# Optimization experiments

Hardware: AMD Instinct MI355X
Metric: run time of the kernel (lower is better)

The kernel has to match this reference:

```python
import jax, jax.numpy as jnp
import numpy as np

SIGMA = 1.0  # init kwarg sigma

def _rbf_kernel(A):
    # K[i,j] = exp(-0.5 * ||a_i - a_j||^2 / sigma^2)
    sq = jnp.sum(A * A, axis=1)                      # [n]
    d2 = sq[:, None] + sq[None, :] - 2.0 * (A @ A.T)  # [n, n]
    return jnp.exp(-0.5 * d2 / (SIGMA ** 2))

def _double_center(K):
    # C K C with C = I - 11^T/n, done in O(n^2) via mean subtraction
    row = K.mean(axis=1, keepdims=True)
    col = K.mean(axis=0, keepdims=True)
    tot = K.mean()
    return K - row - col + tot

def setup_inputs() -> dict:
    key = jax.random.key(0)
    kx, ky = jax.random.split(key)
    X = jax.random.normal(kx, (4096, 512), dtype=jnp.float32)
    Y = jax.random.normal(ky, (4096, 512), dtype=jnp.float32)
    return {"X": X, "Y": Y}

def reference(X, Y):
    n = X.shape[0]
    KXc = _double_center(_rbf_kernel(X))
    KYc = _double_center(_rbf_kernel(Y))
    # trace(KX C KY C) = sum(center(KX) * center(KY)) since K symmetric, C idempotent
    hsic = jnp.sum(KXc * KYc) / ((n - 1) ** 2)
    return hsic
```

## Files before the change

### kernel.cpp

```cpp
#include <hip/hip_runtime.h>
#include <hip/hip_bf16.h>

namespace {

constexpr int N = 4096;
constexpr int D = 512;
constexpr int BM = 64;
constexpr int BK = 64;
constexpr int KITERS = D / BK;
constexpr int NB = N / BM;
constexpr int NBLK = NB * (NB + 1) / 2;
constexpr int TILEB = BM * BK;
constexpr int PANELB = BM * D;

constexpr size_t OFF_XB  = 0;
constexpr size_t OFF_YB  = (size_t)N * D;
constexpr size_t OFF_SQX = OFF_YB + (size_t)N * D;
constexpr size_t OFF_SQY = OFF_SQX + (size_t)N * 4;
constexpr size_t OFF_SX  = OFF_SQY + (size_t)N * 4;
constexpr size_t OFF_SY  = OFF_SX + (size_t)N * 4;
constexpr size_t OFF_T1  = OFF_SY + (size_t)N * 4;
constexpr size_t WS_NEED = OFF_T1 + 4;


constexpr float D2_SKIP = 240.f;

typedef __attribute__((ext_vector_type(4))) float floatx4;
typedef __attribute__((ext_vector_type(2))) long longx2;

__device__ inline void stage16(const void* g, void* l) {
  __builtin_amdgcn_global_load_lds(
      (const __attribute__((address_space(1))) unsigned int*)g,
      (__attribute__((address_space(3))) unsigned int*)l, 16, 0, 0);
}

__device__ inline unsigned short bf16bits(float f) {
  return __builtin_bit_cast(unsigned short, __float2bfloat16(f));
}

__global__ void prep_kernel(const float* __restrict__ X, const float* __restrict__ Y,
                            unsigned char* __restrict__ Xf8, unsigned char* __restrict__ Yf8,
                            float* __restrict__ sqX, float* __restrict__ sqY,
                            float* __restrict__ sX, float* __restrict__ sY,
                            float* __restrict__ T1) {
  const int wave = threadIdx.x >> 6, lane = threadIdx.x & 63;
  const int row = blockIdx.x * 4 + wave;
  const int m = blockIdx.y;
  const float* __restrict__ src = m ? Y : X;
  unsigned char* __restrict__ dst = m ? Yf8 : Xf8;
  float* __restrict__ dsq = m ? sqY : sqX;

  if (threadIdx.x < 4) {
    float* z = m ? sY : sX;
    z[blockIdx.x * 4 + threadIdx.x] = 0.f;
  }
  if (blockIdx.x == 0 && m == 0 && threadIdx.x == 0) *T1 = 0.f;

  const float4* s4 = (const float4*)(src + (size_t)row * D);
  float4 v0 = s4[lane * 2];
  float4 v1 = s4[lane * 2 + 1];
  float acc = v0.x * v0.x + v0.y * v0.y + v0.z * v0.z + v0.w * v0.w
            + v1.x * v1.x + v1.y * v1.y + v1.z * v1.z + v1.w * v1.w;

  unsigned int w0 = 0, w1 = 0;
  w0 = __builtin_amdgcn_cvt_pk_fp8_f32(v0.x, v0.y, w0, false);
  w0 = __builtin_amdgcn_cvt_pk_fp8_f32(v0.z, v0.w, w0, true);
  w1 = __builtin_amdgcn_cvt_pk_fp8_f32(v1.x, v1.y, w1, false);
  w1 = __builtin_amdgcn_cvt_pk_fp8_f32(v1.z, v1.w, w1, true);
  const unsigned long long pk =
      (unsigned long long)w0 | ((unsigned long long)w1 << 32);

  const int p    = row >> 6;
  const int nib  = (row >> 4) & 3;
  const int cl   = row & 15;
  const int ks   = lane >> 3;
  const int pass = (lane >> 2) & 1;
  const int quad = lane & 3;
  const size_t off = (size_t)p * PANELB + (size_t)ks * TILEB +
                     nib * 1024 + quad * 256 + cl * 16 + pass * 8;
  *(unsigned long long*)(dst + off) = pk;

#pragma unroll
  for (int mm = 32; mm >= 1; mm >>= 1) acc += __shfl_xor(acc, mm, 64);
  if (lane == 0) dsq[row] = acc;
}

__launch_bounds__(256, 4)
__global__ void hsic_main(const unsigned char* __restrict__ Xf8,
                          const unsigned char* __restrict__ Yf8,
                          const float* __restrict__ sqX, const float* __restrict__ sqY,
                          float* __restrict__ sX, float* __restrict__ sY,
                          float* __restrict__ T1) {
  __shared__ __align__(16) unsigned char smem[3][2 * TILEB];

  const int b = blockIdx.x;
  int idx = (b & 7) * (NBLK / 8) + (b >> 3);

  const float nf = (float)NB + 0.5f;
  int bI = (int)(nf - sqrtf(nf * nf - 2.0f * (float)idx));
  if (bI < 0) bI = 0;
  if (bI >= NB) bI = NB - 1;
  while (bI * NB - bI * (bI - 1) / 2 > idx) --bI;
  while ((bI + 1) * NB - (bI + 1) * bI / 2 <= idx) ++bI;
  const int bJ = bI + (idx - (bI * NB - bI * (bI - 1) / 2));
  const bool offdiag = (bI != bJ);

  const int tid = threadIdx.x;
  const int lane = tid & 63, wave = tid >> 6;
  const int wm = wave >> 1, wn = wave & 1;
  const int quad = lane >> 4, cl = lane & 15;

  const unsigned char* gAx = Xf8 + (size_t)bI * PANELB;
  const unsigned char* gBx = Xf8 + (size_t)bJ * PANELB;
  const unsigned char* gAy = Yf8 + (size_t)bI * PANELB;
  const unsigned char* gBy = Yf8 + (size_t)bJ * PANELB;

  floatx4 acc[2][2];
#pragma unroll
  for (int i = 0; i < 2; ++i)
#pragma unroll
    for (int j = 0; j < 2; ++j) acc[i][j] = (floatx4){0.f, 0.f, 0.f, 0.f};

  auto stage_all = [&](int iter, int buf) {
    const unsigned char* gA = (iter < KITERS) ? gAx : gAy;
    const unsigned char* gB = (iter < KITERS) ? gBx : gBy;
    const size_t goff = (size_t)(iter & (KITERS - 1)) * TILEB + (size_t)tid * 16;
    stage16(gA + goff, &smem[buf][0 * TILEB + tid * 16]);
    stage16(gB + goff, &smem[buf][1 * TILEB + tid * 16]);
  };

  const int Ib = bI * BM + wm * 32;
  const int Jb = bJ * BM + wn * 32;

  unsigned int kxp[2][2][2];
  unsigned int fmask = 0;
  float t1l = 0.f;

  stage_all(0, 0);
  stage_all(1, 1);

  for (int iter = 0; iter < 2 * KITERS; ++iter) {
    if (iter < 2 * KITERS - 1) {
      asm volatile("s_waitcnt vmcnt(2)" ::: "memory");
    } else {
      asm volatile("s_waitcnt vmcnt(0)" ::: "memory");
    }
    asm volatile("s_barrier" ::: "memory");
    if (iter + 2 < 2 * KITERS) stage_all(iter + 2, (iter + 2) % 3);

    const unsigned char* A = &smem[iter % 3][0];
    const unsigned char* B = &smem[iter % 3][TILEB];

    longx2 bf[2];
#pragma unroll
    for (int ni = 0; ni < 2; ++ni)
      bf[ni] = *(const longx2*)&B[(wn * 2 + ni) * 1024 + (lane << 4)];
#pragma unroll
    for (int mi = 0; mi < 2; ++mi) {
      const longx2 af = *(const longx2*)&A[(wm * 2 + mi) * 1024 + (lane << 4)];
#pragma unroll
      for (int ni = 0; ni < 2; ++ni) {
        acc[mi][ni] = __builtin_amdgcn_mfma_f32_16x16x32_fp8_fp8(af[0], bf[ni][0], acc[mi][ni], 0, 0, 0);
        acc[mi][ni] = __builtin_amdgcn_mfma_f32_16x16x32_fp8_fp8(af[1], bf[ni][1], acc[mi][ni], 0, 0, 0);
      }
    }

    if (iter == KITERS - 1) {
      float rx[2][4];
      float cx[2];
#pragma unroll
      for (int mi = 0; mi < 2; ++mi)
#pragma unroll
        for (int r = 0; r < 4; ++r) rx[mi][r] = 0.f;
#pragma unroll
      for (int ni = 0; ni < 2; ++ni) cx[ni] = 0.f;

#pragma unroll
      for (int mi = 0; mi < 2; ++mi) {
        const int ig0 = Ib + mi * 16 + quad * 4;
        float sxi[4];
#pragma unroll
        for (int r = 0; r < 4; ++r) sxi[r] = sqX[ig0 + r];
#pragma unroll
        for (int ni = 0; ni < 2; ++ni) {
          const int jg = Jb + ni * 16 + cl;
          const float sxj = sqX[jg];
          float d2x[4];
          bool lflag = false;
#pragma unroll
          for (int r = 0; r < 4; ++r) {
            const int ig = ig0 + r;
            d2x[r] = sxi[r] + sxj - 2.f * acc[mi][ni][r];
            lflag |= (d2x[r] < D2_SKIP) | (ig == jg);
          }
          float kxv[4] = {0.f, 0.f, 0.f, 0.f};
          if (__any(lflag)) {
            fmask |= (1u << (mi * 2 + ni));
#pragma unroll
            for (int r = 0; r < 4; ++r) {
              const int ig = ig0 + r;
              kxv[r] = (ig == jg) ? 1.f : __expf(-0.5f * d2x[r]);
              rx[mi][r] += kxv[r];
              cx[ni] += kxv[r];
            }
          }
          kxp[mi][ni][0] = (unsigned)bf16bits(kxv[0]) | ((unsigned)bf16bits(kxv[1]) << 16);
          kxp[mi][ni][1] = (unsigned)bf16bits(kxv[2]) | ((unsigned)bf16bits(kxv[3]) << 16);
          acc[mi][ni] = (floatx4){0.f, 0.f, 0.f, 0.f};
        }
      }

      if (fmask != 0) {
#pragma unroll
        for (int mi = 0; mi < 2; ++mi)
#pragma unroll
          for (int r = 0; r < 4; ++r) {
            float vx = rx[mi][r];
#pragma unroll
            for (int mm = 1; mm < 16; mm <<= 1) vx += __shfl_xor(vx, mm, 16);
            rx[mi][r] = vx;
          }
        if (cl == 0) {
#pragma unroll
          for (int mi = 0; mi < 2; ++mi)
#pragma unroll
            for (int r = 0; r < 4; ++r)
              atomicAdd(&sX[Ib + mi * 16 + quad * 4 + r], rx[mi][r]);
        }
        if (offdiag) {
#pragma unroll
          for (int ni = 0; ni < 2; ++ni) {
            float vx = cx[ni];
            vx += __shfl_xor(vx, 16, 64);
            vx += __shfl_xor(vx, 32, 64);
            if (quad == 0) atomicAdd(&sX[Jb + ni * 16 + cl], vx);
          }
        }
      }
    }
  }

  {
    float ry[2][4];
    float cy[2];
    bool anyy = false;
#pragma unroll
    for (int mi = 0; mi < 2; ++mi)
#pragma unroll
      for (int r = 0; r < 4; ++r) ry[mi][r] = 0.f;
#pragma unroll
    for (int ni = 0; ni < 2; ++ni) cy[ni] = 0.f;

#pragma unroll
    for (int mi = 0; mi < 2; ++mi) {
      const int ig0 = Ib + mi * 16 + quad * 4;
      float syi[4];
#pragma unroll
      for (int r = 0; r < 4; ++r) syi[r] = sqY[ig0 + r];
#pragma unroll
      for (int ni = 0; ni < 2; ++ni) {
        const int jg = Jb + ni * 16 + cl;
        const float syj = sqY[jg];
        float d2y[4];
        bool lflag = false;
#pragma unroll
        for (int r = 0; r < 4; ++r) {
          const int ig = ig0 + r;
          d2y[r] = syi[r] + syj - 2.f * acc[mi][ni][r];
          lflag |= (d2y[r] < D2_SKIP) | (ig == jg);
        }
        const bool xb = (fmask >> (mi * 2 + ni)) & 1u;
        if (__any(lflag) || xb) {
          anyy = true;
          float kyv[4];
#pragma unroll
          for (int r = 0; r < 4; ++r) {
            const int ig = ig0 + r;
            kyv[r] = (ig == jg) ? 1.f : __expf(-0.5f * d2y[r]);
            ry[mi][r] += kyv[r];
            cy[ni] += kyv[r];
          }
          if (xb) {
            const float kx0 = __builtin_bit_cast(float, (kxp[mi][ni][0] & 0xFFFFu) << 16);
            const float kx1 = __builtin_bit_cast(float, kxp[mi][ni][0] & 0xFFFF0000u);
            const float kx2 = __builtin_bit_cast(float, (kxp[mi][ni][1] & 0xFFFFu) << 16);
            const float kx3 = __builtin_bit_cast(float, kxp[mi][ni][1] & 0xFFFF0000u);
            t1l += kx0 * kyv[0] + kx1 * kyv[1] + kx2 * kyv[2] + kx3 * kyv[3];
          }
        }
      }
    }

    if (anyy) {
#pragma unroll
      for (int mi = 0; mi < 2; ++mi)
#pragma unroll
        for (int r = 0; r < 4; ++r) {
          float vy = ry[mi][r];
#pragma unroll
          for (int mm = 1; mm < 16; mm <<= 1) vy += __shfl_xor(vy, mm, 16);
          ry[mi][r] = vy;
        }
      if (cl == 0) {
#pragma unroll
        for (int mi = 0; mi < 2; ++mi)
#pragma unroll
          for (int r = 0; r < 4; ++r)
            atomicAdd(&sY[Ib + mi * 16 + quad * 4 + r], ry[mi][r]);
      }
      if (offdiag) {
#pragma unroll
        for (int ni = 0; ni < 2; ++ni) {
          float vy = cy[ni];
          vy += __shfl_xor(vy, 16, 64);
          vy += __shfl_xor(vy, 32, 64);
          if (quad == 0) atomicAdd(&sY[Jb + ni * 16 + cl], vy);
        }
      }
    }
  }

  if (fmask != 0) {
    t1l *= offdiag ? 2.f : 1.f;
#pragma unroll
    for (int mm = 1; mm < 64; mm <<= 1) t1l += __shfl_xor(t1l, mm, 64);
  }
  __shared__ float tred[4];
  if (lane == 0) tred[wave] = t1l;
  __syncthreads();
  if (tid == 0) {
    const float t = tred[0] + tred[1] + tred[2] + tred[3];
    if (t != 0.f) atomicAdd(T1, t);
  }
}

__global__ void final_kernel(const float* __restrict__ sX, const float* __restrict__ sY,
                             const float* __restrict__ T1, float* __restrict__ out) {
  const int tid = threadIdx.x;
  float dp = 0.f, sa = 0.f, sb = 0.f;
  for (int i = tid; i < N; i += 256) {
    float a = sX[i], b = sY[i];
    dp += a * b; sa += a; sb += b;
  }
#pragma unroll
  for (int mm = 1; mm < 64; mm <<= 1) {
    dp += __shfl_xor(dp, mm, 64);
    sa += __shfl_xor(sa, mm, 64);
    sb += __shfl_xor(sb, mm, 64);
  }
  __shared__ float r0[4], r1[4], r2[4];
  if ((tid & 63) == 0) { int w = tid >> 6; r0[w] = dp; r1[w] = sa; r2[w] = sb; }
  __syncthreads();
  if (tid == 0) {
    dp = r0[0] + r0[1] + r0[2] + r0[3];
    sa = r1[0] + r1[1] + r1[2] + r1[3];
    sb = r2[0] + r2[1] + r2[2] + r2[3];
    const float n = (float)N;
    const float total = T1[0] - (2.f / n) * dp + (sa * sb) / (n * n);
    out[0] = total / ((n - 1.f) * (n - 1.f));
  }
}

}

extern "C" void kernel_launch(void* const* d_in, const int* in_sizes, int n_in,
                              void* d_out, int out_size, void* d_ws, size_t ws_size,
                              hipStream_t stream) {
  const float* X = (const float*)d_in[0];
  const float* Y = (const float*)d_in[1];
  char* ws = (char*)d_ws;
  if (ws_size < WS_NEED) return;

  unsigned char* Xf8 = (unsigned char*)(ws + OFF_XB);
  unsigned char* Yf8 = (unsigned char*)(ws + OFF_YB);
  float* sqX = (float*)(ws + OFF_SQX);
  float* sqY = (float*)(ws + OFF_SQY);
  float* sX  = (float*)(ws + OFF_SX);
  float* sY  = (float*)(ws + OFF_SY);
  float* T1  = (float*)(ws + OFF_T1);
  float* out = (float*)d_out;

  prep_kernel<<<dim3(N / 4, 2), 256, 0, stream>>>(X, Y, Xf8, Yf8, sqX, sqY, sX, sY, T1);
  hsic_main<<<NBLK, 256, 0, stream>>>(Xf8, Yf8, sqX, sqY, sX, sY, T1);
  final_kernel<<<1, 256, 0, stream>>>(sX, sY, T1, out);
}
```

Before: 92.66 us.

## Load fp8 MFMA fragments directly from global memory instead of staging through LDS

Removes the triple-buffered LDS staging with global_load_lds and barriers. Each wave now reads its A and B fragments straight from the pre-swizzled global panels into registers, and the X and Y K-loops are fully unrolled as separate loops. This drops LDS traffic and block-wide synchronisation. In exchange, data shared between the waves of a block is fetched from global/L2 once per wave, and the loads depend on the compiler to schedule them ahead of use.

```diff
diff --git a/kernel.cpp b/kernel.cpp
--- a/kernel.cpp
+++ b/kernel.cpp
@@ -22,17 +22,10 @@
 constexpr size_t OFF_T1  = OFF_SY + (size_t)N * 4;
 constexpr size_t WS_NEED = OFF_T1 + 4;
 
-
 constexpr float D2_SKIP = 240.f;
 
 typedef __attribute__((ext_vector_type(4))) float floatx4;
 typedef __attribute__((ext_vector_type(2))) long longx2;
-
-__device__ inline void stage16(const void* g, void* l) {
-  __builtin_amdgcn_global_load_lds(
-      (const __attribute__((address_space(1))) unsigned int*)g,
-      (__attribute__((address_space(3))) unsigned int*)l, 16, 0, 0);
-}
 
 __device__ inline unsigned short bf16bits(float f) {
   return __builtin_bit_cast(unsigned short, __float2bfloat16(f));
@@ -91,8 +84,6 @@
                           const float* __restrict__ sqX, const float* __restrict__ sqY,
                           float* __restrict__ sX, float* __restrict__ sY,
                           float* __restrict__ T1) {
-  __shared__ __align__(16) unsigned char smem[3][2 * TILEB];
-
   const int b = blockIdx.x;
   int idx = (b & 7) * (NBLK / 8) + (b >> 3);
 
@@ -109,25 +100,18 @@
   const int lane = tid & 63, wave = tid >> 6;
   const int wm = wave >> 1, wn = wave & 1;
   const int quad = lane >> 4, cl = lane & 15;
-
-  const unsigned char* gAx = Xf8 + (size_t)bI * PANELB;
-  const unsigned char* gBx = Xf8 + (size_t)bJ * PANELB;
-  const unsigned char* gAy = Yf8 + (size_t)bI * PANELB;
-  const unsigned char* gBy = Yf8 + (size_t)bJ * PANELB;
+  const int lane16 = lane << 4;
+
+  const unsigned char* gAx = Xf8 + (size_t)bI * PANELB + wm * 2048 + lane16;
+  const unsigned char* gBx = Xf8 + (size_t)bJ * PANELB + wn * 2048 + lane16;
+  const unsigned char* gAy = Yf8 + (size_t)bI * PANELB + wm * 2048 + lane16;
+  const unsigned char* gBy = Yf8 + (size_t)bJ * PANELB + wn * 2048 + lane16;
 
   floatx4 acc[2][2];
 #pragma unroll
   for (int i = 0; i < 2; ++i)
 #pragma unroll
     for (int j = 0; j < 2; ++j) acc[i][j] = (floatx4){0.f, 0.f, 0.f, 0.f};
-
-  auto stage_all = [&](int iter, int buf) {
-    const unsigned char* gA = (iter < KITERS) ? gAx : gAy;
-    const unsigned char* gB = (iter < KITERS) ? gBx : gBy;
-    const size_t goff = (size_t)(iter & (KITERS - 1)) * TILEB + (size_t)tid * 16;
-    stage16(gA + goff, &smem[buf][0 * TILEB + tid * 16]);
-    stage16(gB + goff, &smem[buf][1 * TILEB + tid * 16]);
-  };
 
   const int Ib = bI * BM + wm * 32;
   const int Jb = bJ * BM + wn * 32;
@@ -136,108 +120,114 @@
   unsigned int fmask = 0;
   float t1l = 0.f;
 
-  stage_all(0, 0);
-  stage_all(1, 1);
-
-  for (int iter = 0; iter < 2 * KITERS; ++iter) {
-    if (iter < 2 * KITERS - 1) {
-      asm volatile("s_waitcnt vmcnt(2)" ::: "memory");
-    } else {
-      asm volatile("s_waitcnt vmcnt(0)" ::: "memory");
-    }
-    asm volatile("s_barrier" ::: "memory");
-    if (iter + 2 < 2 * KITERS) stage_all(iter + 2, (iter + 2) % 3);
-
-    const unsigned char* A = &smem[iter % 3][0];
-    const unsigned char* B = &smem[iter % 3][TILEB];
-
-    longx2 bf[2];
+#pragma unroll
+  for (int ks = 0; ks < KITERS; ++ks) {
+    longx2 af[2], bf[2];
+#pragma unroll
+    for (int mi = 0; mi < 2; ++mi)
+      af[mi] = *(const longx2*)(gAx + (size_t)ks * TILEB + mi * 1024);
 #pragma unroll
     for (int ni = 0; ni < 2; ++ni)
-      bf[ni] = *(const longx2*)&B[(wn * 2 + ni) * 1024 + (lane << 4)];
+      bf[ni] = *(const longx2*)(gBx + (size_t)ks * TILEB + ni * 1024);
+#pragma unroll
+    for (int mi = 0; mi < 2; ++mi)
+#pragma unroll
+      for (int ni = 0; ni < 2; ++ni) {
+        acc[mi][ni] = __builtin_amdgcn_mfma_f32_16x16x32_fp8_fp8(af[mi][0], bf[ni][0], acc[mi][ni], 0, 0, 0);
+        acc[mi][ni] = __builtin_amdgcn_mfma_f32_16x16x32_fp8_fp8(af[mi][1], bf[ni][1], acc[mi][ni], 0, 0, 0);
+      }
+  }
+
+  {
+    float rx[2][4];
+    float cx[2];
+#pragma unroll
+    for (int mi = 0; mi < 2; ++mi)
+#pragma unroll
+      for (int r = 0; r < 4; ++r) rx[mi][r] = 0.f;
+#pragma unroll
+    for (int ni = 0; ni < 2; ++ni) cx[ni] = 0.f;
+
 #pragma unroll
     for (int mi = 0; mi < 2; ++mi) {
-      const longx2 af = *(const longx2*)&A[(wm * 2 + mi) * 1024 + (lane << 4)];
+      const int ig0 = Ib + mi * 16 + quad * 4;
+      float sxi[4];
+#pragma unroll
+      for (int r = 0; r < 4; ++r) sxi[r] = sqX[ig0 + r];
 #pragma unroll
       for (int ni = 0; ni < 2; ++ni) {
-        acc[mi][ni] = __builtin_amdgcn_mfma_f32_16x16x32_fp8_fp8(af[0], bf[ni][0], acc[mi][ni], 0, 0, 0);
-        acc[mi][ni] = __builtin_amdgcn_mfma_f32_16x16x32_fp8_fp8(af[1], bf[ni][1], acc[mi][ni], 0, 0, 0);
-      }
-    }
-
-    if (iter == KITERS - 1) {
-      float rx[2][4];
-      float cx[2];
-#pragma unroll
-      for (int mi = 0; mi < 2; ++mi)
-#pragma unroll
-        for (int r = 0; r < 4; ++r) rx[mi][r] = 0.f;
-#pragma unroll
-      for (int ni = 0; ni < 2; ++ni) cx[ni] = 0.f;
-
-#pragma unroll
-      for (int mi = 0; mi < 2; ++mi) {
-        const int ig0 = Ib + mi * 16 + quad * 4;
-        float sxi[4];
-#pragma unroll
-        for (int r = 0; r < 4; ++r) sxi[r] = sqX[ig0 + r];
-#pragma unroll
-        for (int ni = 0; ni < 2; ++ni) {
-          const int jg = Jb + ni * 16 + cl;
-          const float sxj = sqX[jg];
-          float d2x[4];
-          bool lflag = false;
+        const int jg = Jb + ni * 16 + cl;
+        const float sxj = sqX[jg];
+        float d2x[4];
+        bool lflag = false;
+#pragma unroll
+        for (int r = 0; r < 4; ++r) {
+          const int ig = ig0 + r;
+          d2x[r] = sxi[r] + sxj - 2.f * acc[mi][ni][r];
+          lflag |= (d2x[r] < D2_SKIP) | (ig == jg);
+        }
+        float kxv[4] = {0.f, 0.f, 0.f, 0.f};
+        if (__any(lflag)) {
+          fmask |= (1u << (mi * 2 + ni));
 #pragma unroll
           for (int r = 0; r < 4; ++r) {
             const int ig = ig0 + r;
-            d2x[r] = sxi[r] + sxj - 2.f * acc[mi][ni][r];
-            lflag |= (d2x[r] < D2_SKIP) | (ig == jg);
+            kxv[r] = (ig == jg) ? 1.f : __expf(-0.5f * d2x[r]);
+            rx[mi][r] += kxv[r];
+            cx[ni] += kxv[r];
           }
-          float kxv[4] = {0.f, 0.f, 0.f, 0.f};
-          if (__any(lflag)) {
-            fmask |= (1u << (mi * 2 + ni));
-#pragma unroll
-            for (int r = 0; r < 4; ++r) {
-              const int ig = ig0 + r;
-              kxv[r] = (ig == jg) ? 1.f : __expf(-0.5f * d2x[r]);
-              rx[mi][r] += kxv[r];
-              cx[ni] += kxv[r];
-            }
-          }
-          kxp[mi][ni][0] = (unsigned)bf16bits(kxv[0]) | ((unsigned)bf16bits(kxv[1]) << 16);
-          kxp[mi][ni][1] = (unsigned)bf16bits(kxv[2]) | ((unsigned)bf16bits(kxv[3]) << 16);
-          acc[mi][ni] = (floatx4){0.f, 0.f, 0.f, 0.f};
-        }
-      }
-
-      if (fmask != 0) {
+        }
+        kxp[mi][ni][0] = (unsigned)bf16bits(kxv[0]) | ((unsigned)bf16bits(kxv[1]) << 16);
+        kxp[mi][ni][1] = (unsigned)bf16bits(kxv[2]) | ((unsigned)bf16bits(kxv[3]) << 16);
+        acc[mi][ni] = (floatx4){0.f, 0.f, 0.f, 0.f};
+      }
+    }
+
+    if (fmask != 0) {
+#pragma unroll
+      for (int mi = 0; mi < 2; ++mi)
+#pragma unroll
+        for (int r = 0; r < 4; ++r) {
+          float vx = rx[mi][r];
+#pragma unroll
+          for (int mm = 1; mm < 16; mm <<= 1) vx += __shfl_xor(vx, mm, 16);
+          rx[mi][r] = vx;
+        }
+      if (cl == 0) {
 #pragma unroll
         for (int mi = 0; mi < 2; ++mi)
 #pragma unroll
-          for (int r = 0; r < 4; ++r) {
-            float vx = rx[mi][r];
-#pragma unroll
-            for (int mm = 1; mm < 16; mm <<= 1) vx += __shfl_xor(vx, mm, 16);
-            rx[mi][r] = vx;
-          }
-        if (cl == 0) {
-#pragma unroll
-          for (int mi = 0; mi < 2; ++mi)
-#pragma unroll
-            for (int r = 0; r < 4; ++r)
-              atomicAdd(&sX[Ib + mi * 16 + quad * 4 + r], rx[mi][r]);
-        }
-        if (offdiag) {
-#pragma unroll
-          for (int ni = 0; ni < 2; ++ni) {
-            float vx = cx[ni];
-            vx += __shfl_xor(vx, 16, 64);
-            vx += __shfl_xor(vx, 32, 64);
-            if (quad == 0) atomicAdd(&sX[Jb + ni * 16 + cl], vx);
-          }
+          for (int r = 0; r < 4; ++r)
+            atomicAdd(&sX[Ib + mi * 16 + quad * 4 + r], rx[mi][r]);
+      }
+      if (offdiag) {
+#pragma unroll
+        for (int ni = 0; ni < 2; ++ni) {
+          float vx = cx[ni];
+          vx += __shfl_xor(vx, 16, 64);
+          vx += __shfl_xor(vx, 32, 64);
+          if (quad == 0) atomicAdd(&sX[Jb + ni * 16 + cl], vx);
         }
       }
     }
+  }
+
+#pragma unroll
+  for (int ks = 0; ks < KITERS; ++ks) {
+    longx2 af[2], bf[2];
+#pragma unroll
+    for (int mi = 0; mi < 2; ++mi)
+      af[mi] = *(const longx2*)(gAy + (size_t)ks * TILEB + mi * 1024);
+#pragma unroll
+    for (int ni = 0; ni < 2; ++ni)
+      bf[ni] = *(const longx2*)(gBy + (size_t)ks * TILEB + ni * 1024);
+#pragma unroll
+    for (int mi = 0; mi < 2; ++mi)
+#pragma unroll
+      for (int ni = 0; ni < 2; ++ni) {
+        acc[mi][ni] = __builtin_amdgcn_mfma_f32_16x16x32_fp8_fp8(af[mi][0], bf[ni][0], acc[mi][ni], 0, 0, 0);
+        acc[mi][ni] = __builtin_amdgcn_mfma_f32_16x16x32_fp8_fp8(af[mi][1], bf[ni][1], acc[mi][ni], 0, 0, 0);
+      }
   }
 
   {
```

After: 92.06 us. About the same (-0.7%).
